# Optimization experiments

Measured on AMD Instinct MI355X. Metric: run time of the kernel, lower is better.

## Reference

```python
import jax, jax.numpy as jnp
import numpy as np

NUM_HEADS = 8


def setup_inputs() -> dict:
    key = jax.random.key(0)
    ks = jax.random.split(key, 7)
    B, H, W, C = 1, 64, 64, 512
    x = jax.random.normal(ks[0], (B, H, W, C), dtype=jnp.float32)
    # lat in [-pi/2, pi/2), lon in [0, 2*pi) radians
    lat_grid = (jax.random.uniform(ks[1], (H, W), dtype=jnp.float32) - 0.5) * np.float32(np.pi)
    lon_grid = jax.random.uniform(ks[2], (H, W), dtype=jnp.float32) * np.float32(2 * np.pi)
    w_qkv = jax.random.normal(ks[3], (3 * C, C), dtype=jnp.float32) * 0.02
    b_qkv = jax.random.normal(ks[4], (3 * C,), dtype=jnp.float32) * 0.02
    w_out = jax.random.normal(ks[5], (C, C), dtype=jnp.float32) * 0.02
    b_out = jax.random.normal(ks[6], (C,), dtype=jnp.float32) * 0.02
    return {"x": x, "lat_grid": lat_grid, "lon_grid": lon_grid,
            "w_qkv": w_qkv, "b_qkv": b_qkv, "w_out": w_out, "b_out": b_out}


def _distance_bias(lat_grid, lon_grid):
    # Haversine great-circle distance between all pairs of grid points.
    lat = lat_grid.reshape(-1)  # [N]
    lon = lon_grid.reshape(-1)
    dlat = lat[None, :] - lat[:, None]  # [N, N]
    dlon = lon[None, :] - lon[:, None]
    a = jnp.sin(dlat / 2) ** 2 + jnp.cos(lat)[:, None] * jnp.cos(lat)[None, :] * jnp.sin(dlon / 2) ** 2
    dist = 2.0 * jnp.arcsin(jnp.sqrt(jnp.clip(a, 0.0, 1.0)))
    # torch .std() is unbiased (ddof=1)
    return -dist / jnp.std(dist, ddof=1)


def reference(x, lat_grid, lon_grid, w_qkv, b_qkv, w_out, b_out):
    B, H, W, C = x.shape
    nh = NUM_HEADS
    dh = C // nh
    N = H * W
    qkv = x @ w_qkv.T + b_qkv  # [B, H, W, 3C]
    qkv = qkv.reshape(B, N, 3, nh, dh)
    q = jnp.transpose(qkv[:, :, 0], (0, 2, 1, 3))  # [B, nh, N, dh]
    k = jnp.transpose(qkv[:, :, 1], (0, 2, 1, 3))
    v = jnp.transpose(qkv[:, :, 2], (0, 2, 1, 3))
    scale = np.float32(1.0 / np.sqrt(dh))
    attn = jnp.einsum("bhnd,bhmd->bhnm", q, k) * scale  # [B, nh, N, N]
    attn = attn + _distance_bias(lat_grid, lon_grid)[None, None]
    attn = jax.nn.softmax(attn, axis=-1)  # dropout is identity in eval
    out = jnp.einsum("bhnm,bhmd->bhnd", attn, v)  # [B, nh, N, dh]
    out = jnp.transpose(out, (0, 2, 1, 3)).reshape(B, H, W, C)
    return out @ w_out.T + b_out
```

## Files before the change

### kernel.cpp

```cpp
#include <hip/hip_runtime.h>
#include <hip/hip_bf16.h>


typedef __attribute__((ext_vector_type(8))) short bf16x8;
typedef __attribute__((ext_vector_type(4))) float f32x4;

#define MFMA16(a, b, c) __builtin_amdgcn_mfma_f32_16x16x32_bf16(a, b, c, 0, 0, 0)

__device__ __forceinline__ unsigned short f2b(float f) {
    union { float f; unsigned int i; } v;
    v.f = f;
    unsigned int lsb = (v.i >> 16) & 1u;
    unsigned int r = v.i + 0x7fffu + lsb;
    return (unsigned short)(r >> 16);
}

__global__ __launch_bounds__(256) void prep_kernel(
    const float* __restrict__ lat, const float* __restrict__ lon,
    float* __restrict__ dist, double* __restrict__ partials,
    const float* __restrict__ x, unsigned short* __restrict__ xb,
    const float* __restrict__ wq, unsigned short* __restrict__ wqb,
    const float* __restrict__ wo, unsigned short* __restrict__ wob) {
    __shared__ float sl_i[64], sc_i[64], so_i[64];
    __shared__ float sl_j[64], sc_j[64], so_j[64];
    __shared__ double rs[256], rs2[256];

    int b = blockIdx.x;
    int tid = threadIdx.x;

    if (b < 4096) {
        int i0 = (b >> 6) << 6;
        int j0 = (b & 63) << 6;

        if (tid < 64) {
            float la = lat[i0 + tid];
            sl_i[tid] = la; sc_i[tid] = __cosf(la); so_i[tid] = lon[i0 + tid];
        } else if (tid < 128) {
            int t = tid - 64;
            float la = lat[j0 + t];
            sl_j[t] = la; sc_j[t] = __cosf(la); so_j[t] = lon[j0 + t];
        }
        __syncthreads();

        float s = 0.f, s2 = 0.f;
        int col = tid & 63;
        int pcol = ((col & 15) << 2) + (col >> 4);
        float latj = sl_j[col], cj = sc_j[col], lonj = so_j[col];
#pragma unroll
        for (int kk = 0; kk < 16; kk++) {
            int row = (kk << 2) + (tid >> 6);
            float dlat = latj - sl_i[row];
            float dlon = lonj - so_i[row];
            float h1 = __sinf(0.5f * dlat);
            float h2 = __sinf(0.5f * dlon);
            float a = h1 * h1 + sc_i[row] * cj * h2 * h2;
            a = fminf(fmaxf(a, 0.0f), 1.0f);
            float d = 2.0f * asinf(sqrtf(a));
            dist[(size_t)(i0 + row) * 4096 + j0 + pcol] = d;
            s += d;
            s2 += d * d;
        }
        rs[tid] = (double)s; rs2[tid] = (double)s2;
        __syncthreads();
        for (int off = 128; off > 0; off >>= 1) {
            if (tid < off) { rs[tid] += rs[tid + off]; rs2[tid] += rs2[tid + off]; }
            __syncthreads();
        }
        if (tid == 0) {
            partials[2 * b] = rs[0];
            partials[2 * b + 1] = rs2[0];
        }
        return;
    }

    const float* in; unsigned short* out; int t;
    if (b < 5120)      { in = x;  out = xb;  t = (b - 4096) * 256 + tid; }
    else if (b < 5504) { in = wq; out = wqb; t = (b - 5120) * 256 + tid; }
    else               { in = wo; out = wob; t = (b - 5504) * 256 + tid; }
    int l = t & 15, qd = (t >> 4) & 3, c = (t >> 6) & 15, g = t >> 10;
    const float* src = in + ((size_t)g * 16 + l) * 512 + c * 32 + qd * 8;
    float4 v0 = *(const float4*)src;
    float4 v1 = *(const float4*)(src + 4);
    ushort4 u0, u1;
    u0.x = f2b(v0.x); u0.y = f2b(v0.y); u0.z = f2b(v0.z); u0.w = f2b(v0.w);
    u1.x = f2b(v1.x); u1.y = f2b(v1.y); u1.z = f2b(v1.z); u1.w = f2b(v1.w);
    unsigned short* dst = out + (size_t)t * 8;
    *(ushort4*)dst = u0;
    *(ushort4*)(dst + 4) = u1;
}

__global__ __launch_bounds__(256) void qkv_gemm(
    const unsigned short* __restrict__ x, const unsigned short* __restrict__ w,
    const float* __restrict__ b,
    unsigned short* __restrict__ q, unsigned short* __restrict__ k,
    unsigned short* __restrict__ vt,
    const double* __restrict__ partials, float* __restrict__ neg_inv_std) {
    __shared__ unsigned short stage[64][72];
    __shared__ double rs[256], rs2[256];
    int lane = threadIdx.x & 63, wave = threadIdx.x >> 6;
    int l16 = lane & 15, quad = lane >> 4;

    if (blockIdx.x == 24) {
        if (blockIdx.y != 0) return;
        int tid = threadIdx.x;
        double s = 0.0, s2 = 0.0;
        for (int i = tid; i < 4096; i += 256) {
            s += partials[2 * i];
            s2 += partials[2 * i + 1];
        }
        rs[tid] = s; rs2[tid] = s2;
        __syncthreads();
        for (int off = 128; off > 0; off >>= 1) {
            if (tid < off) { rs[tid] += rs[tid + off]; rs2[tid] += rs2[tid + off]; }
            __syncthreads();
        }
        if (tid == 0) {
            double n = 16777216.0;
            double mean = rs[0] / n;
            double var = (rs2[0] - n * mean * mean) / (n - 1.0);
            *neg_inv_std = (float)(-1.0 / sqrt(var));
        }
        return;
    }

    int m0 = blockIdx.y * 64 + wave * 16;
    int n0 = blockIdx.x * 64;

    const unsigned short* abase = x + (size_t)(blockIdx.y * 4 + wave) * 8192 + lane * 8;
    f32x4 acc[4];
#pragma unroll
    for (int nb = 0; nb < 4; nb++) acc[nb] = (f32x4){0.f, 0.f, 0.f, 0.f};

    for (int k0 = 0; k0 < 512; k0 += 32) {
        bf16x8 af = *(const bf16x8*)(abase + (k0 >> 5) * 512);
#pragma unroll
        for (int nb = 0; nb < 4; nb++) {
            bf16x8 bf = *(const bf16x8*)(w + (size_t)((n0 >> 4) + nb) * 8192
                                           + (k0 >> 5) * 512 + lane * 8);
            acc[nb] = MFMA16(af, bf, acc[nb]);
        }
    }
    if (blockIdx.x < 8) {
#pragma unroll
        for (int nb = 0; nb < 4; nb++) {
            int j = n0 + nb * 16 + l16;
            float bj = b[j];
            int h = j >> 6, d = j & 63;
#pragma unroll
            for (int r = 0; r < 4; r++) {
                int n = m0 + quad * 4 + r;
                q[((size_t)h * 4096 + n) * 64 + d] = f2b((acc[nb][r] + bj) * 0.125f);
            }
        }
    } else if (blockIdx.x < 16) {
        int h = blockIdx.x - 8;
#pragma unroll
        for (int nb = 0; nb < 4; nb++) {
            int d = nb * 16 + l16;
            float bj = b[512 + h * 64 + d];
#pragma unroll
            for (int r = 0; r < 4; r++)
                stage[wave * 16 + quad * 4 + r][d] = f2b(acc[nb][r] + bj);
        }
        __syncthreads();
        unsigned short* kb = k + ((size_t)h << 18) + (size_t)blockIdx.y * 4096;
#pragma unroll
        for (int p = 0; p < 2; p++) {
            int rid = p * 256 + threadIdx.x;
            int t = rid >> 7;
            int rem = rid & 127;
            int half = rem >> 6, qd = (rem >> 4) & 3, l = rem & 15;
            const unsigned short* src = &stage[t * 16 + l][half * 32 + qd * 8];
            unsigned short* dst = kb + t * 1024 + half * 512 + qd * 128 + l * 8;
            *(uint4*)dst = *(const uint4*)src;
        }
    } else {
        int h = blockIdx.x - 16;
#pragma unroll
        for (int nb = 0; nb < 4; nb++) {
            int d = nb * 16 + l16;
            float bj = b[1024 + h * 64 + d];
#pragma unroll
            for (int r = 0; r < 4; r++)
                stage[d][quad * 16 + r * 4 + wave] = f2b(acc[nb][r] + bj);
        }
        __syncthreads();
        int t = threadIdx.x;
        int d = t >> 2;
        int nq = (t & 3) * 16;
        unsigned short* dst = vt + ((size_t)h << 18) + (size_t)blockIdx.y * 4096
                            + (d >> 4) * 1024 + ((nq >> 5) & 1) * 512
                            + ((nq >> 3) & 3) * 128 + (d & 15) * 8;
        const unsigned short* src = &stage[d][nq];
        *(uint4*)dst = *(const uint4*)src;
        *(uint4*)(dst + 128) = *(const uint4*)(src + 8);
    }
}

__device__ __forceinline__ void attn_step(
    const unsigned short* __restrict__ kptr, const unsigned short* __restrict__ vtp,
    short* __restrict__ pb, int h, int kv0, int lane, int l16, int quad,
    bf16x8 qf0, bf16x8 qf1, float4 (&dv)[4], const float* __restrict__ drow,
    int kv_next, float nis, f32x4 (&o)[4], float (&lam)[4]) {
    size_t tbase = ((size_t)h << 18) + ((size_t)kv0 << 6) + lane * 8;
    const unsigned short* kb = kptr + tbase;
    const unsigned short* vb = vtp + tbase;
    f32x4 s[4];
    __builtin_amdgcn_s_setprio(1);
#pragma unroll
    for (int cb = 0; cb < 4; cb++) {
        bf16x8 kf0 = *(const bf16x8*)(kb + cb * 1024);
        bf16x8 kf1 = *(const bf16x8*)(kb + cb * 1024 + 512);
        f32x4 z = (f32x4){0.f, 0.f, 0.f, 0.f};
        z = MFMA16(qf0, kf0, z);
        z = MFMA16(qf1, kf1, z);
        s[cb] = z;
    }
    __builtin_amdgcn_s_setprio(0);
    bf16x8 vf[8];
#pragma unroll
    for (int db = 0; db < 4; db++) {
        vf[2 * db]     = *(const bf16x8*)(vb + db * 1024);
        vf[2 * db + 1] = *(const bf16x8*)(vb + db * 1024 + 512);
    }
#pragma unroll
    for (int r = 0; r < 4; r++) {
        s[0][r] = fmaf(dv[r].x, nis, s[0][r]);
        s[1][r] = fmaf(dv[r].y, nis, s[1][r]);
        s[2][r] = fmaf(dv[r].z, nis, s[2][r]);
        s[3][r] = fmaf(dv[r].w, nis, s[3][r]);
    }
#pragma unroll
    for (int r = 0; r < 4; r++)
        dv[r] = *(const float4*)(drow + (size_t)r * 4096 + kv_next);
#pragma unroll
    for (int r = 0; r < 4; r++) {
        float p0 = __expf(s[0][r]);
        float p1 = __expf(s[1][r]);
        float p2 = __expf(s[2][r]);
        float p3 = __expf(s[3][r]);
        lam[r] += (p0 + p1) + (p2 + p3);
        unsigned int w0 = (unsigned int)f2b(p0) | ((unsigned int)f2b(p1) << 16);
        unsigned int w1 = (unsigned int)f2b(p2) | ((unsigned int)f2b(p3) << 16);
        uint2 pk; pk.x = w0; pk.y = w1;
        *(uint2*)(pb + (quad * 4 + r) * 72 + l16 * 4) = pk;
    }
    bf16x8 pf0 = *(const bf16x8*)(pb + l16 * 72 + quad * 8);
    bf16x8 pf1 = *(const bf16x8*)(pb + l16 * 72 + 32 + quad * 8);
    __builtin_amdgcn_s_setprio(1);
#pragma unroll
    for (int db = 0; db < 4; db++) {
        o[db] = MFMA16(pf0, vf[2 * db], o[db]);
        o[db] = MFMA16(pf1, vf[2 * db + 1], o[db]);
    }
    __builtin_amdgcn_s_setprio(0);
}

__global__ __launch_bounds__(512, 4) void attn_kernel(
    const unsigned short* __restrict__ q, const unsigned short* __restrict__ k,
    const unsigned short* __restrict__ vt, const float* __restrict__ dist,
    const float* __restrict__ nis_p, unsigned short* __restrict__ att) {
    __shared__ __align__(16) char smem[18432];
    int tid = threadIdx.x;
    int lane = tid & 63, wave = tid >> 6;
    int l16 = lane & 15, quad = lane >> 4;
    int b = blockIdx.x;
    int xcd = b & 7, j = b >> 3;
    int h  = (xcd & 3) * 2 + (j & 1);
    int qs = (xcd >> 2) * 64 + (j >> 1);
    int qgl = wave & 1;
    int qt = wave >> 1;
    int q0 = qs * 32 + qgl * 16;
    int kvbase = qt * 1024;
    float nis = *nis_p;

    short* pb = (short*)smem + wave * 1152;

    const unsigned short* qbase = q + ((size_t)h * 4096 + q0 + l16) * 64 + quad * 8;
    bf16x8 qf0 = *(const bf16x8*)(qbase);
    bf16x8 qf1 = *(const bf16x8*)(qbase + 32);

    f32x4 o[4];
    float lam[4];
#pragma unroll
    for (int r = 0; r < 4; r++) {
        lam[r] = 0.f;
        o[0][r] = 0.f; o[1][r] = 0.f; o[2][r] = 0.f; o[3][r] = 0.f;
    }

    const float* drow = dist + (size_t)(q0 + quad * 4) * 4096 + l16 * 4;
    float4 dv[4];
#pragma unroll
    for (int r = 0; r < 4; r++)
        dv[r] = *(const float4*)(drow + (size_t)r * 4096 + kvbase);

    for (int it = 0; it < 16; ++it) {
        int kv0 = kvbase + it * 64;
        int kvn = (it == 15) ? kvbase : kv0 + 64;
        attn_step(k, vt, pb, h, kv0, lane, l16, quad, qf0, qf1, dv, drow, kvn,
                  nis, o, lam);
    }

#pragma unroll
    for (int r = 0; r < 4; r++)
#pragma unroll
        for (int off = 1; off < 16; off <<= 1)
            lam[r] += __shfl_xor(lam[r], off, 64);

    __syncthreads();
    float* obuf = (float*)smem;
    float* lbuf = (float*)(smem + 8192);
    if (l16 == 0)
#pragma unroll
        for (int r = 0; r < 4; r++)
            lbuf[qt * 32 + qgl * 16 + quad * 4 + r] = lam[r];
    if (qt == 0) {
#pragma unroll
        for (int db = 0; db < 4; db++)
#pragma unroll
            for (int r = 0; r < 4; r++)
                obuf[(qgl * 16 + quad * 4 + r) * 64 + db * 16 + l16] = o[db][r];
    }
    __syncthreads();
    if (qt == 1) {
#pragma unroll
        for (int db = 0; db < 4; db++)
#pragma unroll
            for (int r = 0; r < 4; r++)
                obuf[(qgl * 16 + quad * 4 + r) * 64 + db * 16 + l16] += o[db][r];
    }
    __syncthreads();
    if (qt == 2) {
#pragma unroll
        for (int db = 0; db < 4; db++)
#pragma unroll
            for (int r = 0; r < 4; r++)
                obuf[(qgl * 16 + quad * 4 + r) * 64 + db * 16 + l16] += o[db][r];
    }
    __syncthreads();
    if (qt == 3) {
#pragma unroll
        for (int db = 0; db < 4; db++)
#pragma unroll
            for (int r = 0; r < 4; r++)
                obuf[(qgl * 16 + quad * 4 + r) * 64 + db * 16 + l16] += o[db][r];
    }
    __syncthreads();

    int rl = tid >> 4;
    int d4 = (tid & 15) * 4;
    float L = lbuf[rl] + lbuf[32 + rl] + lbuf[64 + rl] + lbuf[96 + rl];
    float rinv = 1.0f / L;
    const float* ob = obuf + rl * 64 + d4;
    ushort4 ua;
    ua.x = f2b(ob[0] * rinv); ua.y = f2b(ob[1] * rinv);
    ua.z = f2b(ob[2] * rinv); ua.w = f2b(ob[3] * rinv);
    int row = qs * 32 + rl;
    int col = h * 64 + d4;
    size_t dst = (size_t)(row >> 4) * 8192 + (col >> 5) * 512
               + ((col >> 3) & 3) * 128 + (row & 15) * 8 + (col & 7);
    *(ushort4*)(att + dst) = ua;
}

__global__ __launch_bounds__(256) void out_gemm(
    const unsigned short* __restrict__ att, const unsigned short* __restrict__ w,
    const float* __restrict__ b, float* __restrict__ out) {
    int lane = threadIdx.x & 63, wave = threadIdx.x >> 6;
    int l16 = lane & 15, quad = lane >> 4;
    int m0 = blockIdx.y * 64 + wave * 16;
    int n0 = blockIdx.x * 64;

    const unsigned short* abase = att + (size_t)(blockIdx.y * 4 + wave) * 8192 + lane * 8;
    f32x4 acc[4];
#pragma unroll
    for (int nb = 0; nb < 4; nb++) acc[nb] = (f32x4){0.f, 0.f, 0.f, 0.f};

    for (int k0 = 0; k0 < 512; k0 += 32) {
        bf16x8 af = *(const bf16x8*)(abase + (k0 >> 5) * 512);
#pragma unroll
        for (int nb = 0; nb < 4; nb++) {
            bf16x8 bf = *(const bf16x8*)(w + (size_t)((n0 >> 4) + nb) * 8192
                                           + (k0 >> 5) * 512 + lane * 8);
            acc[nb] = MFMA16(af, bf, acc[nb]);
        }
    }
#pragma unroll
    for (int nb = 0; nb < 4; nb++) {
        float bj = b[n0 + nb * 16 + l16];
#pragma unroll
        for (int r = 0; r < 4; r++)
            out[(size_t)(m0 + quad * 4 + r) * 512 + n0 + nb * 16 + l16] =
                acc[nb][r] + bj;
    }
}

extern "C" void kernel_launch(void* const* d_in, const int* in_sizes, int n_in,
                              void* d_out, int out_size, void* d_ws, size_t ws_size,
                              hipStream_t stream) {
    const float* x    = (const float*)d_in[0];
    const float* lat  = (const float*)d_in[1];
    const float* lon  = (const float*)d_in[2];
    const float* wqkv = (const float*)d_in[3];
    const float* bqkv = (const float*)d_in[4];
    const float* wout = (const float*)d_in[5];
    const float* bout = (const float*)d_in[6];
    float* out = (float*)d_out;

    char* ws = (char*)d_ws;
    float* dist        = (float*)ws;
    double* partials   = (double*)(ws + 67108864);
    float* nis         = (float*)(ws + 67108864 + 65536);
    unsigned short* q  = (unsigned short*)(ws + 67108864 + 65600);
    unsigned short* k  = q  + (size_t)8 * 4096 * 64;
    unsigned short* vt = k  + (size_t)8 * 4096 * 64;
    unsigned short* att = vt + (size_t)8 * 4096 * 64;
    unsigned short* xb  = att + (size_t)4096 * 512;
    unsigned short* wqb = xb  + (size_t)4096 * 512;
    unsigned short* wob = wqb + (size_t)1536 * 512;

    prep_kernel<<<5632, 256, 0, stream>>>(lat, lon, dist, partials,
                                          x, xb, wqkv, wqb, wout, wob);
    qkv_gemm<<<dim3(25, 64), 256, 0, stream>>>(xb, wqb, bqkv, q, k, vt,
                                               partials, nis);
    attn_kernel<<<1024, 512, 0, stream>>>(q, k, vt, dist, nis, att);
    out_gemm<<<dim3(8, 64), 256, 0, stream>>>(att, wob, bout, out);
}
```

Baseline: 216.4 us.

## Compute transposed QK^T so P stays in registers, retile distance bias

The QK^T MFMA operands are swapped so each lane holds scores laid out the way the PV MFMA wants its A operand. That removes the per-step LDS round trip for the probability tile and cuts LDS use. The distance matrix is written in a tiled layout matching the new score layout, so each lane loads its bias with contiguous vector loads. The V staging permutation and the row-sum reduction change to match the new layout. This depends on the operand-layout reasoning being exactly right, and the whole change stands or falls on that.

Result: no change. 218.8 us (+1.1%).

```diff
diff --git a/kernel.cpp b/kernel.cpp
--- a/kernel.cpp
+++ b/kernel.cpp
@@ -44,7 +44,8 @@
 
         float s = 0.f, s2 = 0.f;
         int col = tid & 63;
-        int pcol = ((col & 15) << 2) + (col >> 4);
+        int colpart = ((col >> 4) << 8) + (((col >> 2) & 3) << 6) + (col & 3);
+        size_t tbase = ((size_t)(j0 >> 6) << 10) + colpart;
         float latj = sl_j[col], cj = sc_j[col], lonj = so_j[col];
 #pragma unroll
         for (int kk = 0; kk < 16; kk++) {
@@ -56,7 +57,8 @@
             float a = h1 * h1 + sc_i[row] * cj * h2 * h2;
             a = fminf(fmaxf(a, 0.0f), 1.0f);
             float d = 2.0f * asinf(sqrtf(a));
-            dist[(size_t)(i0 + row) * 4096 + j0 + pcol] = d;
+            dist[tbase + ((size_t)((i0 >> 4) + (row >> 4)) << 16)
+                 + ((row & 15) << 2)] = d;
             s += d;
             s2 += d * d;
         }
@@ -182,7 +184,8 @@
             float bj = b[1024 + h * 64 + d];
 #pragma unroll
             for (int r = 0; r < 4; r++)
-                stage[d][quad * 16 + r * 4 + wave] = f2b(acc[nb][r] + bj);
+                stage[d][quad * 8 + (wave & 1) * 4 + r + (wave >> 1) * 32] =
+                    f2b(acc[nb][r] + bj);
         }
         __syncthreads();
         int t = threadIdx.x;
@@ -199,9 +202,9 @@
 
 __device__ __forceinline__ void attn_step(
     const unsigned short* __restrict__ kptr, const unsigned short* __restrict__ vtp,
-    short* __restrict__ pb, int h, int kv0, int lane, int l16, int quad,
-    bf16x8 qf0, bf16x8 qf1, float4 (&dv)[4], const float* __restrict__ drow,
-    int kv_next, float nis, f32x4 (&o)[4], float (&lam)[4]) {
+    int h, int kv0, int lane,
+    bf16x8 qf0, bf16x8 qf1, f32x4 (&dv)[4], const float* __restrict__ dbase,
+    int kv_next, float nis, f32x4 (&o)[4], float& lam) {
     size_t tbase = ((size_t)h << 18) + ((size_t)kv0 << 6) + lane * 8;
     const unsigned short* kb = kptr + tbase;
     const unsigned short* vb = vtp + tbase;
@@ -212,8 +215,8 @@
         bf16x8 kf0 = *(const bf16x8*)(kb + cb * 1024);
         bf16x8 kf1 = *(const bf16x8*)(kb + cb * 1024 + 512);
         f32x4 z = (f32x4){0.f, 0.f, 0.f, 0.f};
-        z = MFMA16(qf0, kf0, z);
-        z = MFMA16(qf1, kf1, z);
+        z = MFMA16(kf0, qf0, z);
+        z = MFMA16(kf1, qf1, z);
         s[cb] = z;
     }
     __builtin_amdgcn_s_setprio(0);
@@ -224,29 +227,38 @@
         vf[2 * db + 1] = *(const bf16x8*)(vb + db * 1024 + 512);
     }
 #pragma unroll
-    for (int r = 0; r < 4; r++) {
-        s[0][r] = fmaf(dv[r].x, nis, s[0][r]);
-        s[1][r] = fmaf(dv[r].y, nis, s[1][r]);
-        s[2][r] = fmaf(dv[r].z, nis, s[2][r]);
-        s[3][r] = fmaf(dv[r].w, nis, s[3][r]);
-    }
-#pragma unroll
-    for (int r = 0; r < 4; r++)
-        dv[r] = *(const float4*)(drow + (size_t)r * 4096 + kv_next);
-#pragma unroll
-    for (int r = 0; r < 4; r++) {
-        float p0 = __expf(s[0][r]);
-        float p1 = __expf(s[1][r]);
-        float p2 = __expf(s[2][r]);
-        float p3 = __expf(s[3][r]);
-        lam[r] += (p0 + p1) + (p2 + p3);
-        unsigned int w0 = (unsigned int)f2b(p0) | ((unsigned int)f2b(p1) << 16);
-        unsigned int w1 = (unsigned int)f2b(p2) | ((unsigned int)f2b(p3) << 16);
-        uint2 pk; pk.x = w0; pk.y = w1;
-        *(uint2*)(pb + (quad * 4 + r) * 72 + l16 * 4) = pk;
-    }
-    bf16x8 pf0 = *(const bf16x8*)(pb + l16 * 72 + quad * 8);
-    bf16x8 pf1 = *(const bf16x8*)(pb + l16 * 72 + 32 + quad * 8);
+    for (int cb = 0; cb < 4; cb++) {
+        s[cb][0] = fmaf(dv[cb][0], nis, s[cb][0]);
+        s[cb][1] = fmaf(dv[cb][1], nis, s[cb][1]);
+        s[cb][2] = fmaf(dv[cb][2], nis, s[cb][2]);
+        s[cb][3] = fmaf(dv[cb][3], nis, s[cb][3]);
+    }
+    {
+        const float* dnext = dbase + ((size_t)(kv_next >> 6) << 10);
+#pragma unroll
+        for (int cb = 0; cb < 4; cb++)
+            dv[cb] = *(const f32x4*)(dnext + cb * 256);
+    }
+    bf16x8 pf0, pf1;
+#pragma unroll
+    for (int cb = 0; cb < 4; cb++) {
+        float p0 = __expf(s[cb][0]);
+        float p1 = __expf(s[cb][1]);
+        float p2 = __expf(s[cb][2]);
+        float p3 = __expf(s[cb][3]);
+        lam += (p0 + p1) + (p2 + p3);
+        if (cb < 2) {
+            pf0[cb * 4 + 0] = (short)f2b(p0);
+            pf0[cb * 4 + 1] = (short)f2b(p1);
+            pf0[cb * 4 + 2] = (short)f2b(p2);
+            pf0[cb * 4 + 3] = (short)f2b(p3);
+        } else {
+            pf1[(cb - 2) * 4 + 0] = (short)f2b(p0);
+            pf1[(cb - 2) * 4 + 1] = (short)f2b(p1);
+            pf1[(cb - 2) * 4 + 2] = (short)f2b(p2);
+            pf1[(cb - 2) * 4 + 3] = (short)f2b(p3);
+        }
+    }
     __builtin_amdgcn_s_setprio(1);
 #pragma unroll
     for (int db = 0; db < 4; db++) {
@@ -260,7 +272,7 @@
     const unsigned short* __restrict__ q, const unsigned short* __restrict__ k,
     const unsigned short* __restrict__ vt, const float* __restrict__ dist,
     const float* __restrict__ nis_p, unsigned short* __restrict__ att) {
-    __shared__ __align__(16) char smem[18432];
+    __shared__ __align__(16) char smem[8704];
     int tid = threadIdx.x;
     int lane = tid & 63, wave = tid >> 6;
     int l16 = lane & 15, quad = lane >> 4;
@@ -274,46 +286,40 @@
     int kvbase = qt * 1024;
     float nis = *nis_p;
 
-    short* pb = (short*)smem + wave * 1152;
-
     const unsigned short* qbase = q + ((size_t)h * 4096 + q0 + l16) * 64 + quad * 8;
     bf16x8 qf0 = *(const bf16x8*)(qbase);
     bf16x8 qf1 = *(const bf16x8*)(qbase + 32);
 
     f32x4 o[4];
-    float lam[4];
+    float lam = 0.f;
 #pragma unroll
     for (int r = 0; r < 4; r++) {
-        lam[r] = 0.f;
         o[0][r] = 0.f; o[1][r] = 0.f; o[2][r] = 0.f; o[3][r] = 0.f;
     }
 
-    const float* drow = dist + (size_t)(q0 + quad * 4) * 4096 + l16 * 4;
-    float4 dv[4];
-#pragma unroll
-    for (int r = 0; r < 4; r++)
-        dv[r] = *(const float4*)(drow + (size_t)r * 4096 + kvbase);
+    const float* dbase = dist + ((size_t)(q0 >> 4) << 16) + quad * 64 + l16 * 4;
+    f32x4 dv[4];
+    {
+        const float* d0 = dbase + ((size_t)(kvbase >> 6) << 10);
+#pragma unroll
+        for (int cb = 0; cb < 4; cb++)
+            dv[cb] = *(const f32x4*)(d0 + cb * 256);
+    }
 
     for (int it = 0; it < 16; ++it) {
         int kv0 = kvbase + it * 64;
         int kvn = (it == 15) ? kvbase : kv0 + 64;
-        attn_step(k, vt, pb, h, kv0, lane, l16, quad, qf0, qf1, dv, drow, kvn,
-                  nis, o, lam);
-    }
-
-#pragma unroll
-    for (int r = 0; r < 4; r++)
-#pragma unroll
-        for (int off = 1; off < 16; off <<= 1)
-            lam[r] += __shfl_xor(lam[r], off, 64);
+        attn_step(k, vt, h, kv0, lane, qf0, qf1, dv, dbase, kvn, nis, o, lam);
+    }
+
+    lam += __shfl_xor(lam, 16, 64);
+    lam += __shfl_xor(lam, 32, 64);
 
     __syncthreads();
     float* obuf = (float*)smem;
     float* lbuf = (float*)(smem + 8192);
-    if (l16 == 0)
-#pragma unroll
-        for (int r = 0; r < 4; r++)
-            lbuf[qt * 32 + qgl * 16 + quad * 4 + r] = lam[r];
+    if (lane < 16)
+        lbuf[qt * 32 + qgl * 16 + lane] = lam;
     if (qt == 0) {
 #pragma unroll
         for (int db = 0; db < 4; db++)
```
